# Optimization experiments

Hardware: AMD Instinct MI355X
Metric: run time of the kernel (lower is better)

## Reference

```python
import jax, jax.numpy as jnp
import numpy as np
from jax import lax

# pywt 'db6' rec_lo (scaling filter). dec_lo = rec_lo[::-1]; pytorch_wavelets
# stores dec filters flipped for conv (=correlation), so analysis correlation
# filters are exactly rec_lo and rec_hi = qmf(rec_lo). Synthesis filters for
# conv_transpose are rec_lo/rec_hi unflipped -> same arrays.
_DB6 = np.array([0.11154074335008017, 0.4946238903983854, 0.7511339080215775,
                 0.3152503517092432, -0.22626469396516913, -0.12976686756709563,
                 0.09750160558707936, 0.02752286553001629, -0.031582039318031156,
                 0.0005538422009938016, 0.004777257511010651, -0.00107730108499558],
                dtype=np.float32)
_QMF = (_DB6[::-1].copy() * ((-1.0) ** np.arange(12))).astype(np.float32)
H0, H1 = jnp.asarray(_DB6), jnp.asarray(_QMF)
LF, J = 12, 3
BATCH, SEQ_LEN, CH = 128, 720, 321
COMP_L = [99, 365, 188, 99]   # [yl, yh1, yh2, yh3] for seq_len=720
OUT_L = [22, 57, 34, 22]      # same decomposition of red_len=104


def afb1d(x):
    """One-level analysis filter bank, mode='symmetric'. x: [B,C,N]."""
    B, C, N = x.shape
    out = (N + LF - 1) // 2                      # pywt dwt_coeff_len (symmetric)
    p = 2 * (out - 1) - N + LF
    xp = jnp.pad(x, ((0, 0), (0, 0), (p // 2, (p + 1) // 2)), mode='symmetric')
    w = jnp.stack([H0, H1])[:, None, :]          # [2,1,LF]
    y = lax.conv_general_dilated(xp.reshape(B * C, 1, -1), w, (2,), 'VALID',
                                 dimension_numbers=('NCH', 'OIH', 'NCH'))
    y = y.reshape(B, C, 2, out)
    return y[:, :, 0], y[:, :, 1]


def sfb1d(lo, hi):
    """One-level synthesis bank == conv_transpose1d(stride=2, padding=LF-2)."""
    B, C, Lin = lo.shape
    z = jnp.stack([lo, hi], axis=2).reshape(B * C, 2, Lin)
    w = jnp.stack([H0[::-1], H1[::-1]])[None]    # [1,2,LF], flipped for corr
    y = lax.conv_general_dilated(z, w, (1,), ((1, 1),), lhs_dilation=(2,),
                                 dimension_numbers=('NCH', 'OIH', 'NCH'))
    return y.reshape(B, C, -1)                   # length 2*Lin + 2 - LF


def sinusoidal_pe(n_pos, d):
    pos = jnp.arange(n_pos, dtype=jnp.float32)[:, None]
    div = jnp.exp(jnp.arange(0, d, 2, dtype=jnp.float32) * (-np.log(10000.0) / d))
    pe = jnp.zeros((n_pos, d), jnp.float32)
    pe = pe.at[:, 0::2].set(jnp.sin(pos * div))
    pe = pe.at[:, 1::2].set(jnp.cos(pos * div[: d // 2]))
    return pe


def _forward(x, qws, qbs, kws, kbs, pws, pbs, iws, als, bes):
    mean = lax.stop_gradient(jnp.mean(x, axis=1, keepdims=True))
    std = lax.stop_gradient(jnp.sqrt(jnp.var(x, axis=1, keepdims=True) + 1e-5))
    xc = jnp.transpose((x - mean) / std, (0, 2, 1))      # [B,C,L]
    yl, yh = xc, []
    for _ in range(J):
        yl, hi = afb1d(yl)
        yh.append(hi)
    decomps = [yl] + yh                                  # lengths COMP_L
    preds = []
    for i, comp in enumerate(decomps):
        B, C, L = comp.shape
        Q = jnp.tanh(comp @ qws[i].T + qbs[i])           # [B,C,L]
        K = jnp.tanh(comp @ kws[i].T + kbs[i])
        scores = jnp.einsum('bcl,bcs->bls', Q, K) / (L ** 0.5)
        weighted = jnp.mean(jnp.tanh(scores), axis=1)    # [B,S] (equal per channel)
        cum = jnp.flip(jnp.cumsum(jnp.flip(weighted, -1), -1), -1)
        P = jax.nn.softmax(cum * als[i][0], axis=-1)
        idxs = jnp.arange(L, dtype=jnp.float32)
        win = jnp.sum(P * idxs, axis=-1)[:, None, None]  # soft truncation [B,1,1]
        mask = jax.nn.sigmoid((idxs[None, None, :] - win) * bes[i][0])
        pred = (comp * mask) @ pws[i].T + pbs[i]         # [B,C,O]
        pred = jax.nn.softmax(iws[i], axis=1) * (pred + sinusoidal_pe(C, pred.shape[-1])[None])
        preds.append(pred)
    ll = preds[0]
    for h in preds[:0:-1]:                               # coarsest high band first
        if ll.shape[-1] > h.shape[-1]:
            ll = ll[..., : h.shape[-1]]
        ll = sfb1d(ll, h)
    return ll, mean, std


def setup_inputs() -> dict:
    key = jax.random.key(0)
    ks = jax.random.split(key, 64)
    inp = {'x': jax.random.normal(ks[0], (BATCH, SEQ_LEN, CH), jnp.float32)}
    k = 1
    for i, (L, O) in enumerate(zip(COMP_L, OUT_L)):
        s = 1.0 / np.sqrt(L)                             # torch Linear default init
        inp[f'qw{i}'] = jax.random.uniform(ks[k], (L, L), jnp.float32, -s, s); k += 1
        inp[f'qb{i}'] = jax.random.uniform(ks[k], (L,), jnp.float32, -s, s); k += 1
        inp[f'kw{i}'] = jax.random.uniform(ks[k], (L, L), jnp.float32, -s, s); k += 1
        inp[f'kb{i}'] = jax.random.uniform(ks[k], (L,), jnp.float32, -s, s); k += 1
        inp[f'pw{i}'] = jnp.full((O, L), 1.0 / L, jnp.float32)
        inp[f'pb{i}'] = jnp.zeros((O,), jnp.float32)
        inp[f'iw{i}'] = jnp.ones((1, CH, O), jnp.float32)
        inp[f'al{i}'] = jnp.full((1,), 10.0, jnp.float32)
        inp[f'be{i}'] = jnp.full((1,), 10.0, jnp.float32)
    return inp


def reference(x, qw0, qb0, kw0, kb0, pw0, pb0, iw0, al0, be0,
              qw1, qb1, kw1, kb1, pw1, pb1, iw1, al1, be1,
              qw2, qb2, kw2, kb2, pw2, pb2, iw2, al2, be2,
              qw3, qb3, kw3, kb3, pw3, pb3, iw3, al3, be3):
    return _forward(x, [qw0, qw1, qw2, qw3], [qb0, qb1, qb2, qb3],
                    [kw0, kw1, kw2, kw3], [kb0, kb1, kb2, kb3],
                    [pw0, pw1, pw2, pw3], [pb0, pb1, pb2, pb3],
                    [iw0, iw1, iw2, iw3], [al0, al1, al2, al3],
                    [be0, be1, be2, be3])
```

## Files before the change

### kernel.cpp

```cpp
#include <hip/hip_runtime.h>
#include <hip/hip_bf16.h>
#include <math.h>

namespace {
constexpr int kB  = 128;
constexpr int kC  = 321;
constexpr int kN0 = 720;
constexpr int kCp = 384;
}

typedef __attribute__((ext_vector_type(8))) short short8;
typedef __attribute__((ext_vector_type(4))) float floatx4;

__constant__ float c_h0[12] = {
  0.11154074335008017f, 0.4946238903983854f, 0.7511339080215775f,
  0.3152503517092432f, -0.22626469396516913f, -0.12976686756709563f,
  0.09750160558707936f, 0.02752286553001629f, -0.031582039318031156f,
  0.0005538422009938016f, 0.004777257511010651f, -0.00107730108499558f};
__constant__ float c_h1[12] = {
  -0.00107730108499558f, -0.004777257511010651f, 0.0005538422009938016f,
  0.031582039318031156f, 0.02752286553001629f, -0.09750160558707936f,
  -0.12976686756709563f, 0.22626469396516913f, 0.3152503517092432f,
  -0.7511339080215775f, 0.4946238903983854f, -0.11154074335008017f};
__constant__ float c_h0r[12] = {
  -0.00107730108499558f, 0.004777257511010651f, 0.0005538422009938016f,
  -0.031582039318031156f, 0.02752286553001629f, 0.09750160558707936f,
  -0.12976686756709563f, -0.22626469396516913f, 0.3152503517092432f,
  0.7511339080215775f, 0.4946238903983854f, 0.11154074335008017f};
__constant__ float c_h1r[12] = {
  -0.11154074335008017f, 0.4946238903983854f, -0.7511339080215775f,
  0.3152503517092432f, 0.22626469396516913f, -0.12976686756709563f,
  -0.09750160558707936f, 0.02752286553001629f, 0.031582039318031156f,
  0.0005538422009938016f, -0.004777257511010651f, -0.00107730108499558f};

__device__ __forceinline__ float fast_tanh(float x) {
  float e = __expf(2.f * x);
  return 1.f - 2.f / (e + 1.f);
}
__device__ __forceinline__ unsigned short f2b(float f) {
  __hip_bfloat16 h = __float2bfloat16(f);
  return __builtin_bit_cast(unsigned short, h);
}

__global__ void __launch_bounds__(128) partial_ms_kernel(
    const float* __restrict__ x, float* __restrict__ ps, float* __restrict__ ps2) {
  int b = blockIdx.x, chunk = blockIdx.y;
  int c = blockIdx.z * 128 + threadIdx.x;
  if (c >= kC) return;
  const float* xb = x + (size_t)b * kN0 * kC + c;
  int t0 = chunk * 90;
  float s = 0.f, s2 = 0.f;
#pragma unroll 15
  for (int i = 0; i < 90; ++i) {
    float v = xb[(size_t)(t0 + i) * kC];
    s += v; s2 += v * v;
  }
  ps [(b * 8 + chunk) * kC + c] = s;
  ps2[(b * 8 + chunk) * kC + c] = s2;
}

__global__ void __launch_bounds__(256) finalize_ms_kernel(
    const float* __restrict__ ps, const float* __restrict__ ps2,
    float* __restrict__ mout, float* __restrict__ sout,
    float* __restrict__ meanw, float* __restrict__ invw) {
  int i = blockIdx.x * 256 + threadIdx.x;
  if (i >= kB * kC) return;
  int b = i / kC, c = i - b * kC;
  float s = 0.f, s2 = 0.f;
#pragma unroll
  for (int k = 0; k < 8; ++k) { s += ps[(b * 8 + k) * kC + c]; s2 += ps2[(b * 8 + k) * kC + c]; }
  float mean = s * (1.f / (float)kN0);
  float var = s2 * (1.f / (float)kN0) - mean * mean;
  float sd = sqrtf(var + 1e-5f);
  mout[i] = mean; sout[i] = sd;
  meanw[i] = mean; invw[i] = 1.f / sd;
}

__device__ __forceinline__ int sym_reflect(int t, int N) {
  t = (t < 0) ? (-1 - t) : t;
  t = (t >= N) ? (2 * N - 1 - t) : t;
  return t;
}

template <bool NORM, bool LO_F32, bool LO_BF16>
__global__ void __launch_bounds__(256) dwt_fused_kernel(
    const float* __restrict__ in, const float* __restrict__ meanw,
    const float* __restrict__ invw, float* __restrict__ loF,
    unsigned short* __restrict__ loB, unsigned short* __restrict__ hiB,
    int N, int L, int Lp) {
  __shared__ float xs[138][64];
  __shared__ unsigned short los[64][72];
  __shared__ unsigned short his[64][72];
  const int b = blockIdx.z;
  const int n0 = blockIdx.x * 64, c0 = blockIdx.y * 64;
  const int tid = threadIdx.x;
  const int cl = tid & 63, wv = tid >> 6;
  const int c = c0 + cl;
  const int t0 = 2 * n0 - 10;
  const float* ib = in + (size_t)b * N * kC;
  float mean = 0.f, inv = 1.f;
  if (NORM && c < kC) { mean = meanw[b * kC + c]; inv = invw[b * kC + c]; }
  for (int r = wv; r < 138; r += 4) {
    int t = sym_reflect(t0 + r, N);
    float v = (c < kC) ? ib[(size_t)t * kC + c] : 0.f;
    if (NORM) v = (v - mean) * inv;
    xs[r][cl] = v;
  }
  __syncthreads();
#pragma unroll 4
  for (int k = 0; k < 16; ++k) {
    int nl = wv + 4 * k;
    int n = n0 + nl;
    float a0 = 0.f, a1 = 0.f;
    int base = 2 * nl;
#pragma unroll
    for (int j = 0; j < 12; ++j) {
      float v = xs[base + j][cl];
      a0 += v * c_h0[j]; a1 += v * c_h1[j];
    }
    bool valid = (n < L) && (c < kC);
    if (LO_F32 && valid) loF[((size_t)b * L + n) * kC + c] = a0;
    if (LO_BF16) los[cl][nl] = f2b(valid ? a0 : 0.f);
    his[cl][nl] = f2b(valid ? a1 : 0.f);
  }
  __syncthreads();
  int row = tid >> 2, part = tid & 3;
  size_t dst = ((size_t)b * kCp + c0 + row) * Lp + n0 + part * 16;
  *(uint4*)(hiB + dst)     = *(const uint4*)&his[row][part * 16];
  *(uint4*)(hiB + dst + 8) = *(const uint4*)&his[row][part * 16 + 8];
  if (LO_BF16) {
    *(uint4*)(loB + dst)     = *(const uint4*)&los[row][part * 16];
    *(uint4*)(loB + dst + 8) = *(const uint4*)&los[row][part * 16 + 8];
  }
}

struct WcArgs { const float* src[8]; unsigned short* dst[8]; int L[8]; int Lp[8]; };
__global__ void __launch_bounds__(256) wconv_all_kernel(WcArgs a) {
  int lvl = blockIdx.y;
  int Lp = a.Lp[lvl], L = a.L[lvl];
  int i = blockIdx.x * 256 + threadIdx.x;
  if (i >= Lp * Lp) return;
  int p = i / Lp, l = i - p * Lp;
  a.dst[lvl][i] = f2b((p < L && l < L) ? a.src[lvl][(size_t)p * L + l] : 0.f);
}

struct QKAllArgs {
  const unsigned short* W[8];
  const unsigned short* Xt[4];
  const float* bias[8];
  unsigned short* Y[8];
  int Lp[4], L[4], yOff[4];
};
__global__ void __launch_bounds__(256) qk_all_kernel(QKAllArgs a) {
  const int y = blockIdx.y;
  const int lvl = (y >= a.yOff[1]) + (y >= a.yOff[2]) + (y >= a.yOff[3]);
  const int Lp = a.Lp[lvl], L = a.L[lvl];
  const int rel = y - a.yOff[lvl];
  const int pt = Lp >> 7;
  const int sel = rel / pt;
  const int pBase = (rel - sel * pt) * 128;
  const unsigned short* Wb = a.W[2 * lvl + sel] + (size_t)pBase * Lp;
  const float* bias = a.bias[2 * lvl + sel];
  unsigned short* Yd = a.Y[2 * lvl + sel];
  const int b = blockIdx.z;
  const int cBase = blockIdx.x * 128;
  const int tid = threadIdx.x;
  const int ln = tid & 63, w = tid >> 6;
  const int wm = w & 1, wn = w >> 1;
  __shared__ short As[128 * 72];
  __shared__ short Bs[128 * 72];
  floatx4 acc[4][4] = {};
  const unsigned short* Xb = a.Xt[lvl] + ((size_t)b * kCp + cBase) * Lp;
  const int kIters = Lp >> 6;
  for (int kt = 0; kt < kIters; ++kt) {
    const int lc = kt << 6;
#pragma unroll
    for (int q = 0; q < 4; ++q) {
      int id = q * 256 + tid;
      int row = id >> 3, pos = (id & 7) * 8;
      *(uint4*)&As[row * 72 + pos] = *(const uint4*)(Wb + (size_t)row * Lp + lc + pos);
      *(uint4*)&Bs[row * 72 + pos] = *(const uint4*)(Xb + (size_t)row * Lp + lc + pos);
    }
    __syncthreads();
#pragma unroll
    for (int sub = 0; sub < 2; ++sub) {
      short8 av[4], bv[4];
#pragma unroll
      for (int mi = 0; mi < 4; ++mi)
        av[mi] = *(const short8*)&As[(wm * 64 + mi * 16 + (ln & 15)) * 72 + (ln >> 4) * 8 + sub * 32];
#pragma unroll
      for (int ni = 0; ni < 4; ++ni)
        bv[ni] = *(const short8*)&Bs[(wn * 64 + ni * 16 + (ln & 15)) * 72 + (ln >> 4) * 8 + sub * 32];
#pragma unroll
      for (int mi = 0; mi < 4; ++mi)
#pragma unroll
        for (int ni = 0; ni < 4; ++ni)
          acc[mi][ni] = __builtin_amdgcn_mfma_f32_16x16x32_bf16(av[mi], bv[ni], acc[mi][ni], 0, 0, 0);
    }
    __syncthreads();
  }
#pragma unroll
  for (int mi = 0; mi < 4; ++mi) {
#pragma unroll
    for (int r = 0; r < 4; ++r) {
      int p = pBase + wm * 64 + mi * 16 + (ln >> 4) * 4 + r;
      float bv = (p < L) ? bias[p] : 0.f;
#pragma unroll
      for (int ni = 0; ni < 4; ++ni) {
        int c = cBase + wn * 64 + ni * 16 + (ln & 15);
        float v = (p < L && c < kC) ? fast_tanh(acc[mi][ni][r] + bv) : 0.f;
        Yd[((size_t)b * Lp + p) * kCp + c] = f2b(v);
      }
    }
  }
}

struct ScAllArgs {
  const unsigned short* Q[4]; const unsigned short* K[4];
  float* wgt[4];
  int Lp[4], L[4], tOff[4];
  float scale[4];
};
__global__ void __launch_bounds__(256) scores_all_kernel(ScAllArgs a) {
  const int t = blockIdx.x;
  const int lvl = (t >= a.tOff[1]) + (t >= a.tOff[2]) + (t >= a.tOff[3]);
  const int rel = t - a.tOff[lvl];
  const int Lp = a.Lp[lvl], L = a.L[lvl];
  const int pt = Lp >> 7;
  const int sBase = (rel % pt) * 128;
  const int lBase = (rel / pt) * 128;
  const int b = blockIdx.y;
  const int tid = threadIdx.x;
  const int ln = tid & 63, w = tid >> 6;
  const int wm = w & 1, wn = w >> 1;
  __shared__ short As[128 * 72];
  __shared__ short Bs[128 * 72];
  __shared__ float red[128];
  floatx4 acc[4][4] = {};
  const unsigned short* Qp = a.Q[lvl] + ((size_t)b * Lp + lBase) * kCp;
  const unsigned short* Kp = a.K[lvl] + ((size_t)b * Lp + sBase) * kCp;
  for (int cc = 0; cc < kCp; cc += 64) {
#pragma unroll
    for (int q = 0; q < 4; ++q) {
      int id = q * 256 + tid;
      int row = id >> 3, pos = (id & 7) * 8;
      *(uint4*)&As[row * 72 + pos] = *(const uint4*)(Qp + (size_t)row * kCp + cc + pos);
      *(uint4*)&Bs[row * 72 + pos] = *(const uint4*)(Kp + (size_t)row * kCp + cc + pos);
    }
    __syncthreads();
#pragma unroll
    for (int sub = 0; sub < 2; ++sub) {
      short8 av[4], bv[4];
#pragma unroll
      for (int mi = 0; mi < 4; ++mi)
        av[mi] = *(const short8*)&As[(wm * 64 + mi * 16 + (ln & 15)) * 72 + (ln >> 4) * 8 + sub * 32];
#pragma unroll
      for (int ni = 0; ni < 4; ++ni)
        bv[ni] = *(const short8*)&Bs[(wn * 64 + ni * 16 + (ln & 15)) * 72 + (ln >> 4) * 8 + sub * 32];
#pragma unroll
      for (int mi = 0; mi < 4; ++mi)
#pragma unroll
        for (int ni = 0; ni < 4; ++ni)
          acc[mi][ni] = __builtin_amdgcn_mfma_f32_16x16x32_bf16(av[mi], bv[ni], acc[mi][ni], 0, 0, 0);
    }
    __syncthreads();
  }
  if (tid < 128) red[tid] = 0.f;
  __syncthreads();
  const float scale = a.scale[lvl];
#pragma unroll
  for (int ni = 0; ni < 4; ++ni) {
    float p = 0.f;
#pragma unroll
    for (int mi = 0; mi < 4; ++mi)
#pragma unroll
      for (int r = 0; r < 4; ++r) p += fast_tanh(acc[mi][ni][r] * scale);
    p += __shfl_xor(p, 16);
    p += __shfl_xor(p, 32);
    if ((ln & 48) == 0) atomicAdd(&red[wn * 64 + ni * 16 + (ln & 15)], p);
  }
  __syncthreads();
  if (tid < 128) {
    int s = sBase + tid;
    if (s < L) atomicAdd(&a.wgt[lvl][(size_t)b * L + s], red[tid]);
  }
}

struct WinArgs { const float* wgt[4]; const float* al[4]; const float* be[4];
                 float* mask[4]; int L[4]; };
__global__ void __launch_bounds__(64) winmask_all_kernel(WinArgs a) {
  int lvl = blockIdx.y;
  int b = blockIdx.x, lane = threadIdx.x;
  int L = a.L[lvl];
  const float* wgt = a.wgt[lvl] + (size_t)b * L;
  float al = a.al[lvl][0], be = a.be[lvl][0];
  float invL = 1.f / (float)L;
  int chunk = (L + 63) >> 6;
  int s0 = lane * chunk;
  float v[6];
  float csum = 0.f;
  for (int i = chunk - 1; i >= 0; --i) {
    int s = s0 + i;
    float xv = (s < L) ? wgt[s] * invL : 0.f;
    csum += xv; v[i] = csum;
  }
  float tot = csum;
  for (int o = 1; o < 64; o <<= 1) {
    float t = __shfl_down(tot, o);
    if (lane + o < 64) tot += t;
  }
  float excl = tot - csum;
  float m = -1e30f;
  for (int i = 0; i < chunk; ++i)
    if (s0 + i < L) m = fmaxf(m, al * (v[i] + excl));
  for (int o = 32; o; o >>= 1) m = fmaxf(m, __shfl_xor(m, o));
  float sum = 0.f, num = 0.f;
  for (int i = 0; i < chunk; ++i) {
    int s = s0 + i;
    if (s < L) { float e = __expf(al * (v[i] + excl) - m); sum += e; num += e * (float)s; }
  }
  for (int o = 32; o; o >>= 1) { sum += __shfl_xor(sum, o); num += __shfl_xor(num, o); }
  float win = num / sum;
  float* mk = a.mask[lvl] + (size_t)b * L;
  for (int i = 0; i < chunk; ++i) {
    int s = s0 + i;
    if (s < L) mk[s] = 1.f / (1.f + __expf(-((float)s - win) * be));
  }
}

struct IwArgs { const float* iw[4]; float* sm[4]; int O[4]; };
__global__ void __launch_bounds__(64) iwsm_all_kernel(IwArgs a) {
  int x = blockIdx.x;
  int lvl, o;
  if (x < 22) { lvl = 0; o = x; }
  else if (x < 79) { lvl = 1; o = x - 22; }
  else if (x < 113) { lvl = 2; o = x - 79; }
  else { lvl = 3; o = x - 113; }
  int O = a.O[lvl];
  const float* iw = a.iw[lvl];
  int lane = threadIdx.x;
  float m = -1e30f;
  for (int c = lane; c < kC; c += 64) m = fmaxf(m, iw[c * O + o]);
  for (int k = 32; k; k >>= 1) m = fmaxf(m, __shfl_xor(m, k));
  float sum = 0.f;
  for (int c = lane; c < kC; c += 64) sum += __expf(iw[c * O + o] - m);
  for (int k = 32; k; k >>= 1) sum += __shfl_xor(sum, k);
  float inv = 1.f / sum;
  for (int c = lane; c < kC; c += 64) a.sm[lvl][c * O + o] = __expf(iw[c * O + o] - m) * inv;
}

struct PredAllArgs {
  const unsigned short* Xt[4];
  const float* PW[4]; const float* PB[4]; const float* MK[4]; const float* SM[4];
  float* OUT[4];
  int L[4], Lp[4], O[4];
};
__global__ void __launch_bounds__(256) pred_all_kernel(PredAllArgs a) {
  const int lvl = blockIdx.y;
  const int L = a.L[lvl], Lp = a.Lp[lvl], O = a.O[lvl];
  const float* PW = a.PW[lvl];
  const int b = blockIdx.z;
  const int cBase = blockIdx.x * 128;
  const int tid = threadIdx.x;
  const int ln = tid & 63, w = tid >> 6;
  __shared__ short As[64 * 40];
  __shared__ short Bs[128 * 40];
  floatx4 acc[8] = {};
  const unsigned short* Xb = a.Xt[lvl] + ((size_t)b * kCp + cBase) * Lp;
  const float* mk = a.MK[lvl] + (size_t)b * L;
  for (int lc = 0; lc < Lp; lc += 32) {
    {
      int o = tid >> 2, j0 = (tid & 3) * 8;
      alignas(16) unsigned short tmp[8];
#pragma unroll
      for (int j = 0; j < 8; ++j) {
        int l = lc + j0 + j;
        float v = (o < O && l < L) ? PW[(size_t)o * L + l] * mk[l] : 0.f;
        tmp[j] = f2b(v);
      }
      *(uint4*)&As[o * 40 + j0] = *(const uint4*)tmp;
    }
#pragma unroll
    for (int q = 0; q < 2; ++q) {
      int ch = tid * 2 + q;
      int row = ch >> 2, pos = ch & 3;
      *(uint4*)(&Bs[row * 40 + pos * 8]) = *(const uint4*)(Xb + (size_t)row * Lp + lc + pos * 8);
    }
    __syncthreads();
    short8 av = *(const short8*)&As[(w * 16 + (ln & 15)) * 40 + (ln >> 4) * 8];
#pragma unroll
    for (int ni = 0; ni < 8; ++ni) {
      short8 bb = *(const short8*)&Bs[(ni * 16 + (ln & 15)) * 40 + (ln >> 4) * 8];
      acc[ni] = __builtin_amdgcn_mfma_f32_16x16x32_bf16(av, bb, acc[ni], 0, 0, 0);
    }
    __syncthreads();
  }
  const float negln = -logf(10000.f) / (float)O;
#pragma unroll
  for (int ni = 0; ni < 8; ++ni) {
    int c = cBase + ni * 16 + (ln & 15);
    if (c >= kC) continue;
#pragma unroll
    for (int r = 0; r < 4; ++r) {
      int o = w * 16 + (ln >> 4) * 4 + r;
      if (o >= O) continue;
      float dv = __expf(negln * (float)(2 * (o >> 1)));
      float ang = (float)c * dv;
      float pe = (o & 1) ? cosf(ang) : sinf(ang);
      a.OUT[lvl][((size_t)b * O + o) * kC + c] = a.SM[lvl][c * O + o] * (acc[ni][r] + a.PB[lvl][o] + pe);
    }
  }
}

__global__ void __launch_bounds__(256) sfb_fused_kernel(
    const float* __restrict__ P0, const float* __restrict__ P1,
    const float* __restrict__ P2, const float* __restrict__ P3,
    float* __restrict__ out) {
  __shared__ float p0s[22][32], p3s[22][32], p2s[34][32], p1s[57][32];
  __shared__ float r1s[34][32], r2s[58][32];
  __shared__ float outs[104][33];
  int b = blockIdx.y, c0 = blockIdx.x * 32;
  int tid = threadIdx.x;
  int cl = tid & 31, r = tid >> 5;
  int c = c0 + cl;
  bool cv = c < kC;
  for (int o = r; o < 22; o += 8) {
    p0s[o][cl] = cv ? P0[((size_t)b * 22 + o) * kC + c] : 0.f;
    p3s[o][cl] = cv ? P3[((size_t)b * 22 + o) * kC + c] : 0.f;
  }
  for (int o = r; o < 34; o += 8) p2s[o][cl] = cv ? P2[((size_t)b * 34 + o) * kC + c] : 0.f;
  for (int o = r; o < 57; o += 8) p1s[o][cl] = cv ? P1[((size_t)b * 57 + o) * kC + c] : 0.f;
  __syncthreads();
  for (int n = r; n < 34; n += 8) {
    float acc = 0.f;
#pragma unroll
    for (int j = 0; j < 12; ++j) {
      int m = n + j - 1;
      if (m < 0 || (m & 1)) continue;
      int i = m >> 1;
      if (i >= 22) continue;
      acc += c_h0r[j] * p0s[i][cl] + c_h1r[j] * p3s[i][cl];
    }
    r1s[n][cl] = acc;
  }
  __syncthreads();
  for (int n = r; n < 58; n += 8) {
    float acc = 0.f;
#pragma unroll
    for (int j = 0; j < 12; ++j) {
      int m = n + j - 1;
      if (m < 0 || (m & 1)) continue;
      int i = m >> 1;
      if (i >= 34) continue;
      acc += c_h0r[j] * r1s[i][cl] + c_h1r[j] * p2s[i][cl];
    }
    r2s[n][cl] = acc;
  }
  __syncthreads();
  for (int n = r; n < 104; n += 8) {
    float acc = 0.f;
#pragma unroll
    for (int j = 0; j < 12; ++j) {
      int m = n + j - 1;
      if (m < 0 || (m & 1)) continue;
      int i = m >> 1;
      if (i >= 57) continue;
      acc += c_h0r[j] * r2s[i][cl] + c_h1r[j] * p1s[i][cl];
    }
    outs[n][cl] = acc;
  }
  __syncthreads();
  for (int idx = tid; idx < 32 * 104; idx += 256) {
    int ci = idx / 104, n = idx - ci * 104;
    int cg = c0 + ci;
    if (cg < kC) out[((size_t)b * kC + cg) * 104 + n] = outs[n][ci];
  }
}

extern "C" void kernel_launch(void* const* d_in, const int* in_sizes, int n_in,
                              void* d_out, int out_size, void* d_ws, size_t ws_size,
                              hipStream_t stream) {
  (void)in_sizes; (void)n_in; (void)out_size; (void)ws_size;
  const float* x = (const float*)d_in[0];
  auto inp = [&](int lvl, int j) { return (const float*)d_in[1 + 9 * lvl + j]; };

  float* outf = (float*)d_out;
  float* mout = outf + (size_t)kB * kC * 104;
  float* sout = mout + (size_t)kB * kC;

  float* Wp = (float*)d_ws;
  size_t off = 0;
  auto alloc = [&](size_t n) { float* p = Wp + off; off += (n + 63) & ~(size_t)63; return p; };

  float* LO1 = alloc((size_t)kB * 365 * kC);
  float* LO2 = alloc((size_t)kB * 188 * kC);
  unsigned short* Xt1 = (unsigned short*)alloc((size_t)kB * kCp * 384 / 2);
  unsigned short* Xt2 = (unsigned short*)alloc((size_t)kB * kCp * 256 / 2);
  unsigned short* Xt0 = (unsigned short*)alloc((size_t)kB * kCp * 128 / 2);
  unsigned short* Xt3 = (unsigned short*)alloc((size_t)kB * kCp * 128 / 2);
  unsigned short* KbfAll = (unsigned short*)alloc((size_t)kB * kCp * 896 / 2);
  unsigned short* Wpv[8];
  for (int i = 0; i < 8; ++i)
    Wpv[i] = (unsigned short*)alloc((size_t)384 * 384 / 2);
  float* wgtAll = alloc((size_t)kB * (99 + 365 + 188 + 99));
  float* M0 = alloc((size_t)kB * 99);  float* M1 = alloc((size_t)kB * 365);
  float* M2 = alloc((size_t)kB * 188); float* M3 = alloc((size_t)kB * 99);
  float* S0 = alloc((size_t)kC * 22);  float* S1 = alloc((size_t)kC * 57);
  float* S2 = alloc((size_t)kC * 34);  float* S3 = alloc((size_t)kC * 22);
  float* P0 = alloc((size_t)kB * 22 * kC); float* P1 = alloc((size_t)kB * 57 * kC);
  float* P2 = alloc((size_t)kB * 34 * kC); float* P3 = alloc((size_t)kB * 22 * kC);
  float* ps   = alloc((size_t)kB * 8 * kC);
  float* ps2  = alloc((size_t)kB * 8 * kC);
  float* meanw = alloc((size_t)kB * kC);
  float* invw  = alloc((size_t)kB * kC);
  unsigned short* QbfAll = (unsigned short*)LO1;

  const int Lc[4]  = {99, 365, 188, 99};
  const int Lpv[4] = {128, 384, 256, 128};
  const int Ov[4]  = {22, 57, 34, 22};
  const int prefLp[4] = {0, 128, 512, 768};
  const int wOff[4] = {0, 99, 99 + 365, 99 + 365 + 188};
  unsigned short* Qlvl[4]; unsigned short* Klvl[4];
  for (int i = 0; i < 4; ++i) {
    Qlvl[i] = QbfAll + (size_t)kB * kCp * prefLp[i];
    Klvl[i] = KbfAll + (size_t)kB * kCp * prefLp[i];
  }
  const unsigned short* Xts[4] = {Xt0, Xt1, Xt2, Xt3};
  float* masks[4] = {M0, M1, M2, M3};
  float* smws[4]  = {S0, S1, S2, S3};
  float* preds[4] = {P0, P1, P2, P3};

  partial_ms_kernel<<<dim3(kB, 8, 3), 128, 0, stream>>>(x, ps, ps2);
  finalize_ms_kernel<<<(kB * kC + 255) / 256, 256, 0, stream>>>(ps, ps2, mout, sout, meanw, invw);

  dwt_fused_kernel<true, true, false><<<dim3(6, kCp / 64, kB), 256, 0, stream>>>(
      x, meanw, invw, LO1, nullptr, Xt1, kN0, 365, 384);
  dwt_fused_kernel<false, true, false><<<dim3(4, kCp / 64, kB), 256, 0, stream>>>(
      LO1, nullptr, nullptr, LO2, nullptr, Xt2, 365, 188, 256);
  dwt_fused_kernel<false, false, true><<<dim3(2, kCp / 64, kB), 256, 0, stream>>>(
      LO2, nullptr, nullptr, nullptr, Xt0, Xt3, 188, 99, 128);

  {
    WcArgs wa;
    for (int i = 0; i < 4; ++i) {
      wa.src[2 * i] = inp(i, 0); wa.src[2 * i + 1] = inp(i, 2);
      wa.dst[2 * i] = Wpv[2 * i]; wa.dst[2 * i + 1] = Wpv[2 * i + 1];
      wa.L[2 * i] = wa.L[2 * i + 1] = Lc[i];
      wa.Lp[2 * i] = wa.Lp[2 * i + 1] = Lpv[i];
    }
    wconv_all_kernel<<<dim3(576, 8), 256, 0, stream>>>(wa);
  }
  hipMemsetAsync(wgtAll, 0, (size_t)kB * (99 + 365 + 188 + 99) * sizeof(float), stream);

  {
    QKAllArgs qa;
    for (int i = 0; i < 4; ++i) {
      qa.W[2 * i] = Wpv[2 * i]; qa.W[2 * i + 1] = Wpv[2 * i + 1];
      qa.bias[2 * i] = inp(i, 1); qa.bias[2 * i + 1] = inp(i, 3);
      qa.Y[2 * i] = Qlvl[i]; qa.Y[2 * i + 1] = Klvl[i];
      qa.Xt[i] = Xts[i]; qa.Lp[i] = Lpv[i]; qa.L[i] = Lc[i];
    }
    qa.yOff[0] = 0; qa.yOff[1] = 2; qa.yOff[2] = 8; qa.yOff[3] = 12;
    qk_all_kernel<<<dim3(kCp / 128, 14, kB), 256, 0, stream>>>(qa);
  }

  {
    ScAllArgs sa;
    for (int i = 0; i < 4; ++i) {
      sa.Q[i] = Qlvl[i]; sa.K[i] = Klvl[i];
      sa.wgt[i] = wgtAll + (size_t)kB * wOff[i];
      sa.Lp[i] = Lpv[i]; sa.L[i] = Lc[i];
      sa.scale[i] = 1.0f / sqrtf((float)Lc[i]);
    }
    sa.tOff[0] = 0; sa.tOff[1] = 1; sa.tOff[2] = 10; sa.tOff[3] = 14;
    scores_all_kernel<<<dim3(15, kB), 256, 0, stream>>>(sa);
  }

  {
    WinArgs wa;
    for (int i = 0; i < 4; ++i) {
      wa.wgt[i] = wgtAll + (size_t)kB * wOff[i];
      wa.al[i] = inp(i, 7); wa.be[i] = inp(i, 8);
      wa.mask[i] = masks[i]; wa.L[i] = Lc[i];
    }
    winmask_all_kernel<<<dim3(kB, 4), 64, 0, stream>>>(wa);
    IwArgs ia;
    for (int i = 0; i < 4; ++i) { ia.iw[i] = inp(i, 6); ia.sm[i] = smws[i]; ia.O[i] = Ov[i]; }
    iwsm_all_kernel<<<135, 64, 0, stream>>>(ia);
  }

  {
    PredAllArgs pa;
    for (int i = 0; i < 4; ++i) {
      pa.Xt[i] = Xts[i]; pa.PW[i] = inp(i, 4); pa.PB[i] = inp(i, 5);
      pa.MK[i] = masks[i]; pa.SM[i] = smws[i]; pa.OUT[i] = preds[i];
      pa.L[i] = Lc[i]; pa.Lp[i] = Lpv[i]; pa.O[i] = Ov[i];
    }
    pred_all_kernel<<<dim3(kCp / 128, 4, kB), 256, 0, stream>>>(pa);
  }

  sfb_fused_kernel<<<dim3(11, kB), 256, 0, stream>>>(P0, P1, P2, P3, outf);
}
```

Measured before the change: 854.2 us.

## Fuse Q/K projections per block and use direct global-to-LDS loads with XOR swizzle

The QK projection kernel now computes both the Q and K outputs in one block, sharing the staged X tile across two weight tiles. This halves the grid and the X reloads. Both the QK and scores kernels replace register-staged global loads with global_load_lds direct-to-LDS transfers into an unpadded, XOR-swizzled shared layout, which avoids bank conflicts and the VGPR round trip. The trade-off is doubled accumulator registers per thread, which may lower occupancy, and fewer blocks per launch.

```diff
diff --git a/kernel.cpp b/kernel.cpp
--- a/kernel.cpp
+++ b/kernel.cpp
@@ -40,6 +40,12 @@
 __device__ __forceinline__ unsigned short f2b(float f) {
   __hip_bfloat16 h = __float2bfloat16(f);
   return __builtin_bit_cast(unsigned short, h);
+}
+
+__device__ __forceinline__ void gload16(const unsigned short* g, short* l) {
+  __builtin_amdgcn_global_load_lds(
+      (const __attribute__((address_space(1))) unsigned int*)g,
+      (__attribute__((address_space(3))) unsigned int*)l, 16, 0, 0);
 }
 
 __global__ void __launch_bounds__(128) partial_ms_kernel(
@@ -155,61 +161,76 @@
   const int y = blockIdx.y;
   const int lvl = (y >= a.yOff[1]) + (y >= a.yOff[2]) + (y >= a.yOff[3]);
   const int Lp = a.Lp[lvl], L = a.L[lvl];
-  const int rel = y - a.yOff[lvl];
-  const int pt = Lp >> 7;
-  const int sel = rel / pt;
-  const int pBase = (rel - sel * pt) * 128;
-  const unsigned short* Wb = a.W[2 * lvl + sel] + (size_t)pBase * Lp;
-  const float* bias = a.bias[2 * lvl + sel];
-  unsigned short* Yd = a.Y[2 * lvl + sel];
+  const int pBase = (y - a.yOff[lvl]) * 128;
+  const unsigned short* W0 = a.W[2 * lvl]     + (size_t)pBase * Lp;
+  const unsigned short* W1 = a.W[2 * lvl + 1] + (size_t)pBase * Lp;
   const int b = blockIdx.z;
   const int cBase = blockIdx.x * 128;
   const int tid = threadIdx.x;
   const int ln = tid & 63, w = tid >> 6;
   const int wm = w & 1, wn = w >> 1;
-  __shared__ short As[128 * 72];
-  __shared__ short Bs[128 * 72];
-  floatx4 acc[4][4] = {};
+  __shared__ short Aq[128 * 64];
+  __shared__ short Ak[128 * 64];
+  __shared__ short Bs[128 * 64];
+  floatx4 acc[2][4][4] = {};
   const unsigned short* Xb = a.Xt[lvl] + ((size_t)b * kCp + cBase) * Lp;
   const int kIters = Lp >> 6;
+  const int srow = w * 32;
+  const int lrow = ln >> 3, lslot = ln & 7;
+  const int gswz = (lslot ^ lrow) << 3;
+  const int sc0 = (((ln >> 4) + 0) ^ (ln & 7)) << 3;
+  const int sc1 = (((ln >> 4) + 4) ^ (ln & 7)) << 3;
   for (int kt = 0; kt < kIters; ++kt) {
     const int lc = kt << 6;
 #pragma unroll
     for (int q = 0; q < 4; ++q) {
-      int id = q * 256 + tid;
-      int row = id >> 3, pos = (id & 7) * 8;
-      *(uint4*)&As[row * 72 + pos] = *(const uint4*)(Wb + (size_t)row * Lp + lc + pos);
-      *(uint4*)&Bs[row * 72 + pos] = *(const uint4*)(Xb + (size_t)row * Lp + lc + pos);
+      const int row = srow + 8 * q + lrow;
+      const size_t goff = (size_t)row * Lp + lc + gswz;
+      short* ldst = (short*)&Aq[(srow + 8 * q) * 64];
+      gload16(W0 + goff, ldst);
+      gload16(W1 + goff, ldst + 128 * 64);
+      gload16(Xb + goff, ldst + 2 * 128 * 64);
     }
     __syncthreads();
 #pragma unroll
     for (int sub = 0; sub < 2; ++sub) {
-      short8 av[4], bv[4];
+      const int sc = sub ? sc1 : sc0;
+      short8 a0[4], a1[4], bv[4];
+#pragma unroll
+      for (int mi = 0; mi < 4; ++mi) {
+        const int ar = (wm * 64 + mi * 16 + (ln & 15)) * 64 + sc;
+        a0[mi] = *(const short8*)&Aq[ar];
+        a1[mi] = *(const short8*)&Ak[ar];
+      }
+#pragma unroll
+      for (int ni = 0; ni < 4; ++ni)
+        bv[ni] = *(const short8*)&Bs[(wn * 64 + ni * 16 + (ln & 15)) * 64 + sc];
 #pragma unroll
       for (int mi = 0; mi < 4; ++mi)
-        av[mi] = *(const short8*)&As[(wm * 64 + mi * 16 + (ln & 15)) * 72 + (ln >> 4) * 8 + sub * 32];
-#pragma unroll
-      for (int ni = 0; ni < 4; ++ni)
-        bv[ni] = *(const short8*)&Bs[(wn * 64 + ni * 16 + (ln & 15)) * 72 + (ln >> 4) * 8 + sub * 32];
-#pragma unroll
-      for (int mi = 0; mi < 4; ++mi)
-#pragma unroll
-        for (int ni = 0; ni < 4; ++ni)
-          acc[mi][ni] = __builtin_amdgcn_mfma_f32_16x16x32_bf16(av[mi], bv[ni], acc[mi][ni], 0, 0, 0);
+#pragma unroll
+        for (int ni = 0; ni < 4; ++ni) {
+          acc[0][mi][ni] = __builtin_amdgcn_mfma_f32_16x16x32_bf16(a0[mi], bv[ni], acc[0][mi][ni], 0, 0, 0);
+          acc[1][mi][ni] = __builtin_amdgcn_mfma_f32_16x16x32_bf16(a1[mi], bv[ni], acc[1][mi][ni], 0, 0, 0);
+        }
     }
     __syncthreads();
   }
 #pragma unroll
-  for (int mi = 0; mi < 4; ++mi) {
-#pragma unroll
-    for (int r = 0; r < 4; ++r) {
-      int p = pBase + wm * 64 + mi * 16 + (ln >> 4) * 4 + r;
-      float bv = (p < L) ? bias[p] : 0.f;
-#pragma unroll
-      for (int ni = 0; ni < 4; ++ni) {
-        int c = cBase + wn * 64 + ni * 16 + (ln & 15);
-        float v = (p < L && c < kC) ? fast_tanh(acc[mi][ni][r] + bv) : 0.f;
-        Yd[((size_t)b * Lp + p) * kCp + c] = f2b(v);
+  for (int s = 0; s < 2; ++s) {
+    const float* bias = a.bias[2 * lvl + s];
+    unsigned short* Yd = a.Y[2 * lvl + s];
+#pragma unroll
+    for (int mi = 0; mi < 4; ++mi) {
+#pragma unroll
+      for (int r = 0; r < 4; ++r) {
+        int p = pBase + wm * 64 + mi * 16 + (ln >> 4) * 4 + r;
+        float bv = (p < L) ? bias[p] : 0.f;
+#pragma unroll
+        for (int ni = 0; ni < 4; ++ni) {
+          int c = cBase + wn * 64 + ni * 16 + (ln & 15);
+          float v = (p < L && c < kC) ? fast_tanh(acc[s][mi][ni][r] + bv) : 0.f;
+          Yd[((size_t)b * Lp + p) * kCp + c] = f2b(v);
+        }
       }
     }
   }
@@ -233,30 +254,37 @@
   const int tid = threadIdx.x;
   const int ln = tid & 63, w = tid >> 6;
   const int wm = w & 1, wn = w >> 1;
-  __shared__ short As[128 * 72];
-  __shared__ short Bs[128 * 72];
+  __shared__ short As[128 * 64];
+  __shared__ short Bs[128 * 64];
   __shared__ float red[128];
   floatx4 acc[4][4] = {};
   const unsigned short* Qp = a.Q[lvl] + ((size_t)b * Lp + lBase) * kCp;
   const unsigned short* Kp = a.K[lvl] + ((size_t)b * Lp + sBase) * kCp;
+  const int srow = w * 32;
+  const int lrow = ln >> 3, lslot = ln & 7;
+  const int gswz = (lslot ^ lrow) << 3;
+  const int sc0 = (((ln >> 4) + 0) ^ (ln & 7)) << 3;
+  const int sc1 = (((ln >> 4) + 4) ^ (ln & 7)) << 3;
   for (int cc = 0; cc < kCp; cc += 64) {
 #pragma unroll
     for (int q = 0; q < 4; ++q) {
-      int id = q * 256 + tid;
-      int row = id >> 3, pos = (id & 7) * 8;
-      *(uint4*)&As[row * 72 + pos] = *(const uint4*)(Qp + (size_t)row * kCp + cc + pos);
-      *(uint4*)&Bs[row * 72 + pos] = *(const uint4*)(Kp + (size_t)row * kCp + cc + pos);
+      const int row = srow + 8 * q + lrow;
+      const size_t goff = (size_t)row * kCp + cc + gswz;
+      short* ldst = (short*)&As[(srow + 8 * q) * 64];
+      gload16(Qp + goff, ldst);
+      gload16(Kp + goff, ldst + 128 * 64);
     }
     __syncthreads();
 #pragma unroll
     for (int sub = 0; sub < 2; ++sub) {
+      const int sc = sub ? sc1 : sc0;
       short8 av[4], bv[4];
 #pragma unroll
       for (int mi = 0; mi < 4; ++mi)
-        av[mi] = *(const short8*)&As[(wm * 64 + mi * 16 + (ln & 15)) * 72 + (ln >> 4) * 8 + sub * 32];
+        av[mi] = *(const short8*)&As[(wm * 64 + mi * 16 + (ln & 15)) * 64 + sc];
 #pragma unroll
       for (int ni = 0; ni < 4; ++ni)
-        bv[ni] = *(const short8*)&Bs[(wn * 64 + ni * 16 + (ln & 15)) * 72 + (ln >> 4) * 8 + sub * 32];
+        bv[ni] = *(const short8*)&Bs[(wn * 64 + ni * 16 + (ln & 15)) * 64 + sc];
 #pragma unroll
       for (int mi = 0; mi < 4; ++mi)
 #pragma unroll
@@ -560,8 +588,8 @@
       qa.Y[2 * i] = Qlvl[i]; qa.Y[2 * i + 1] = Klvl[i];
       qa.Xt[i] = Xts[i]; qa.Lp[i] = Lpv[i]; qa.L[i] = Lc[i];
     }
-    qa.yOff[0] = 0; qa.yOff[1] = 2; qa.yOff[2] = 8; qa.yOff[3] = 12;
-    qk_all_kernel<<<dim3(kCp / 128, 14, kB), 256, 0, stream>>>(qa);
+    qa.yOff[0] = 0; qa.yOff[1] = 1; qa.yOff[2] = 4; qa.yOff[3] = 6;
+    qk_all_kernel<<<dim3(kCp / 128, 7, kB), 256, 0, stream>>>(qa);
   }
 
   {
```

After: 865.4 us. About the same (+1.3%).
